# Kernel tuning notes

Measured on AMD Instinct MI355X. Metric: run time of the kernel, lower is better.

The kernel has to match this reference:

```python
import jax, jax.numpy as jnp
import numpy as np
from jax import lax

EPS = 1e-20  # matches sample_gumbel eps in the TF source


def setup_inputs() -> dict:
    key = jax.random.key(0)
    ks = jax.random.split(key, 7)
    B, T, D, H, K = 32, 512, 512, 512, 64
    x = jax.random.normal(ks[0], (B, T, D), jnp.float32)
    f_after = jax.random.normal(ks[1], (K, D, H), jnp.float32) * 0.02
    f_skip = jax.random.normal(ks[2], (2 * H, 2), jnp.float32) * 0.05
    gru_kernel = jax.random.normal(ks[3], (D, 3 * H), jnp.float32) * 0.02
    gru_rec_kernel = jax.random.normal(ks[4], (H, 3 * H), jnp.float32) * 0.02
    gru_bias = jnp.zeros((2, 3 * H), jnp.float32)
    u_gumbel = jax.random.uniform(ks[5], (T, B, 2), jnp.float32)
    return {"x": x, "f_after": f_after, "f_skip": f_skip,
            "gru_kernel": gru_kernel, "gru_rec_kernel": gru_rec_kernel,
            "gru_bias": gru_bias, "u_gumbel": u_gumbel}


def reference(x, f_after, f_skip, gru_kernel, gru_rec_kernel, gru_bias, u_gumbel):
    # z_after = tanh(conv1d(x, f_after, SAME))  -> [B, T, H]
    z_after = lax.conv_general_dilated(
        x, f_after, window_strides=(1,), padding='SAME',
        dimension_numbers=('NWC', 'WIO', 'NWC'))
    z_after = jnp.tanh(z_after)

    # gumbel(0,1) noise from uniform draws, per step: [T, B, 2]
    g = -jnp.log(-jnp.log(u_gumbel + EPS) + EPS)

    b_in, b_rec = gru_bias[0], gru_bias[1]  # reset_after=True biases, each [3H]
    H = gru_rec_kernel.shape[0]
    B = x.shape[0]
    h0 = jnp.zeros((B, H), x.dtype)

    xs = (jnp.swapaxes(x, 0, 1), jnp.swapaxes(z_after, 0, 1), g)  # time-major

    def step(h_prev, inp):
        x_t, za_t, g_t = inp
        # skip gate: concat(h_{t-1}, z_after_t) @ f_skip, gumbel-softmax (temp=1)
        logits = jnp.concatenate([h_prev, za_t], axis=-1) @ f_skip  # [B, 2]
        skip = jax.nn.softmax(logits + g_t, axis=-1)
        # Keras GRUCell (reset_after=True), gate order z, r, h
        xm = x_t @ gru_kernel + b_in          # [B, 3H]
        hm = h_prev @ gru_rec_kernel + b_rec  # [B, 3H]
        xz, xr, xh = jnp.split(xm, 3, axis=-1)
        hz, hr, hh = jnp.split(hm, 3, axis=-1)
        z = jax.nn.sigmoid(xz + hz)
        r = jax.nn.sigmoid(xr + hr)
        hc = jnp.tanh(xh + r * hh)
        ht = z * h_prev + (1.0 - z) * hc
        # skip blend
        ht = skip[:, 0:1] * h_prev + skip[:, 1:2] * ht
        return ht, ht

    _, ys = lax.scan(step, h0, xs)           # [T, B, H]
    return jnp.swapaxes(ys, 0, 1)            # [B, T, H]
```

## Files before the change

kernel.cpp:

```cpp
#include <hip/hip_runtime.h>
#include <stdint.h>

typedef unsigned short u16;
typedef unsigned int   u32;
typedef __attribute__((ext_vector_type(8))) short short8;
typedef __attribute__((ext_vector_type(4))) float f32x4;
typedef __attribute__((ext_vector_type(4))) u32   u32x4;

#define AS1 __attribute__((address_space(1)))
#define AS3 __attribute__((address_space(3)))

#define SENT 0x7FC0u
#define HS   528

__device__ __forceinline__ float bf2f(u16 u) {
  union { u32 i; float f; } v; v.i = ((u32)u) << 16; return v.f;
}
__device__ __forceinline__ u16 f2bf(float f) {
  union { float f; u32 i; } v; v.f = f;
  u32 i = v.i;
  i += 0x7FFFu + ((i >> 16) & 1u);
  return (u16)(i >> 16);
}
__device__ __forceinline__ float tanh_fast(float x) {
  const float e = __expf(-2.f * fabsf(x));
  const float t = (1.f - e) / (1.f + e);
  return __builtin_copysignf(t, x);
}

__device__ __forceinline__ void gload16(const u16* src, u16* ldsDst) {
  __builtin_amdgcn_global_load_lds((const AS1 u32*)src, (AS3 u32*)ldsDst, 16, 0, 0);
}

__device__ __forceinline__ short8 ldg_sc_h_wait(const u16* p) {
  short8 r;
  asm volatile("global_load_dwordx4 %0, %1, off sc0 sc1\n\t"
               "s_waitcnt vmcnt(0)"
               : "=v"(r) : "v"(p) : "memory");
  return r;
}
__device__ __forceinline__ void stg_sc_h(u16* p, u16 v) {
  asm volatile("global_store_short %0, %1, off sc0 sc1" :: "v"(p), "v"((u32)v) : "memory");
}

__global__ void k_init(const float* __restrict__ x, u16* __restrict__ xp) {
  const long NXP = 32L * 576 * 512;
  long i0 = (long)blockIdx.x * 256 + threadIdx.x;
  for (long i = i0; i < NXP; i += (long)gridDim.x * 256) {
    long b = i / (576 * 512);
    int rem = (int)(i - b * (576 * 512));
    int rr = rem >> 9, dd = rem & 511;
    int t = rr - 31;
    float v = (t >= 0 && t < 512) ? x[(b * 512 + t) * 512 + dd] : 0.f;
    xp[i] = f2bf(v);
  }
}

__global__ void k_sent(u32* __restrict__ hs) {
  const u32x4 s = u32x4{(SENT << 16) | SENT, (SENT << 16) | SENT,
                        (SENT << 16) | SENT, (SENT << 16) | SENT};
  *(u32x4*)&hs[((long)blockIdx.x * 256 + threadIdx.x) * 4] = s;
}

__global__ void k_transpose_cast(const float* __restrict__ in, u16* __restrict__ out,
                                 int rows, int cols, long inWStride, long outWStride) {
  __shared__ float tile[64][65];
  const int w = blockIdx.z;
  const float* ip = in + (long)w * inWStride;
  u16* op = out + (long)w * outWStride;
  const int r0 = blockIdx.y * 64, c0 = blockIdx.x * 64;
  const int tr = threadIdx.x >> 6, tc = threadIdx.x & 63;
  #pragma unroll
  for (int p = 0; p < 16; ++p) {
    int rr = p * 4 + tr;
    tile[rr][tc] = ip[(long)(r0 + rr) * cols + c0 + tc];
  }
  __syncthreads();
  #pragma unroll
  for (int p = 0; p < 16; ++p) {
    int rr = p * 4 + tr;
    op[(long)(c0 + rr) * rows + r0 + tc] = f2bf(tile[tc][rr]);
  }
}

__global__ __launch_bounds__(256) void k_conv(
    const u16* __restrict__ A, const u16* __restrict__ Bm, u16* __restrict__ C)
{
  __shared__ __align__(16) u16 Abig[192 * 64];
  __shared__ __align__(16) u16 Blds[128 * 64];
  const int bid0 = blockIdx.x;
  const int bid = (bid0 & 7) * 64 + (bid0 >> 3);
  const int mt = bid & 127, nt = bid >> 7;
  const int bb = (mt * 128) >> 9;
  const int t0 = (mt * 128) & 511;
  const int h0 = nt * 128;
  const int tid = threadIdx.x;
  const int wv = tid >> 6, l = tid & 63;
  const int wr = wv >> 1, wc = wv & 1;
  const int sRow = wv * 8 + (l >> 3);
  const int sCol = (l & 7) * 8;
  f32x4 acc[4][4];
  #pragma unroll
  for (int m = 0; m < 4; ++m)
    #pragma unroll
    for (int n = 0; n < 4; ++n) acc[m][n] = f32x4{0.f, 0.f, 0.f, 0.f};

  const long aRow0 = (long)(bb * 576 + t0);
  for (int dsub = 0; dsub < 8; ++dsub) {
    const int dcol = dsub << 6;
    for (int w = 0; w < 64; ++w) {
      __syncthreads();
      if (w == 0) {
        #pragma unroll
        for (int c = 0; c < 6; ++c)
          gload16(A + (aRow0 + c * 32 + sRow) * 512 + dcol + sCol,
                  &Abig[(c * 32 + wv * 8) * 64]);
      }
      #pragma unroll
      for (int c = 0; c < 4; ++c)
        gload16(Bm + ((long)w << 18) + (long)(h0 + c * 32 + sRow) * 512 + dcol + sCol,
                &Blds[(c * 32 + wv * 8) * 64]);
      __syncthreads();
      #pragma unroll
      for (int kk = 0; kk < 2; ++kk) {
        short8 af[4], bf[4];
        #pragma unroll
        for (int m = 0; m < 4; ++m)
          af[m] = *(const short8*)&Abig[(w + wr * 64 + m * 16 + (l & 15)) * 64 + kk * 32 + (l >> 4) * 8];
        #pragma unroll
        for (int n = 0; n < 4; ++n)
          bf[n] = *(const short8*)&Blds[(wc * 64 + n * 16 + (l & 15)) * 64 + kk * 32 + (l >> 4) * 8];
        #pragma unroll
        for (int m = 0; m < 4; ++m)
          #pragma unroll
          for (int n = 0; n < 4; ++n)
            acc[m][n] = __builtin_amdgcn_mfma_f32_16x16x32_bf16(af[m], bf[n], acc[m][n], 0, 0, 0);
      }
    }
  }
  const int lr = (l >> 4) * 4, lc = l & 15;
  #pragma unroll
  for (int m = 0; m < 4; ++m)
    #pragma unroll
    for (int n = 0; n < 4; ++n)
      #pragma unroll
      for (int r = 0; r < 4; ++r) {
        const int row = mt * 128 + wr * 64 + m * 16 + lr + r;
        const int col = h0 + wc * 64 + n * 16 + lc;
        C[(long)row * 512 + col] = f2bf(tanhf(acc[m][n][r]));
      }
}

__global__ __launch_bounds__(256) void k_gemm(
    const u16* __restrict__ A, const u16* __restrict__ Bm, u16* __restrict__ C,
    int nTiles, int kw, int woff, long bWStride, int outMode)
{
  __shared__ __align__(16) u16 Alds[128 * 64];
  __shared__ __align__(16) u16 Blds[128 * 64];
  const int bid0 = blockIdx.x;
  const int cpx = gridDim.x >> 3;
  const int bid = (bid0 & 7) * cpx + (bid0 >> 3);
  const int mt = bid / nTiles, nt = bid - mt * nTiles;
  const int bb = (mt * 128) >> 9;
  const int t0 = (mt * 128) & 511;
  const int h0 = nt * 128;
  const int tid = threadIdx.x;
  const int wv = tid >> 6, l = tid & 63;
  const int wr = wv >> 1, wc = wv & 1;
  const int sRow = wv * 8 + (l >> 3);
  const int sCol = (l & 7) * 8;
  f32x4 acc[4][4];
  #pragma unroll
  for (int m = 0; m < 4; ++m)
    #pragma unroll
    for (int n = 0; n < 4; ++n) acc[m][n] = f32x4{0.f, 0.f, 0.f, 0.f};

  const int kIters = kw * 8;
  const long aRow0 = (long)(bb * 576 + t0 + woff);
  for (int q = 0; q < kIters; ++q) {
    const int w = q >> 3, dsub = (q & 7) << 6;
    const u16* aB = A + (aRow0 + w) * 512 + dsub + sCol;
    const u16* bB = Bm + (long)w * bWStride + (long)h0 * 512 + dsub + sCol;
    __syncthreads();
    #pragma unroll
    for (int c = 0; c < 4; ++c) {
      gload16(aB + (long)(c * 32 + sRow) * 512, &Alds[c * 2048 + wv * 512]);
      gload16(bB + (long)(c * 32 + sRow) * 512, &Blds[c * 2048 + wv * 512]);
    }
    __syncthreads();
    #pragma unroll
    for (int kk = 0; kk < 2; ++kk) {
      short8 af[4], bf[4];
      #pragma unroll
      for (int m = 0; m < 4; ++m)
        af[m] = *(const short8*)&Alds[(wr * 64 + m * 16 + (l & 15)) * 64 + kk * 32 + (l >> 4) * 8];
      #pragma unroll
      for (int n = 0; n < 4; ++n)
        bf[n] = *(const short8*)&Blds[(wc * 64 + n * 16 + (l & 15)) * 64 + kk * 32 + (l >> 4) * 8];
      #pragma unroll
      for (int m = 0; m < 4; ++m)
        #pragma unroll
        for (int n = 0; n < 4; ++n)
          acc[m][n] = __builtin_amdgcn_mfma_f32_16x16x32_bf16(af[m], bf[n], acc[m][n], 0, 0, 0);
    }
  }
  const int lr = (l >> 4) * 4, lc = l & 15;
  #pragma unroll
  for (int m = 0; m < 4; ++m)
    #pragma unroll
    for (int n = 0; n < 4; ++n)
      #pragma unroll
      for (int r = 0; r < 4; ++r) {
        const int row = mt * 128 + wr * 64 + m * 16 + lr + r;
        const int col = h0 + wc * 64 + n * 16 + lc;
        const float v = acc[m][n][r];
        if (outMode == 0) {
          C[(long)row * 512 + col] = f2bf(tanhf(v));
        } else {
          const int b = row >> 9, t = row & 511;
          C[((long)t * 32 + b) * 1536 + col] = f2bf(v);
        }
      }
}

__global__ void k_dza(const u16* __restrict__ za, const float* __restrict__ fskip,
                      const float* __restrict__ ug, float* __restrict__ dza) {
  __shared__ float wd2[512];
  const int t = blockIdx.x, tid = threadIdx.x;
  for (int i = tid; i < 512; i += 256) wd2[i] = fskip[(512 + i) * 2 + 1] - fskip[(512 + i) * 2];
  __syncthreads();
  const int b = tid >> 3, seg = (tid & 7) * 64;
  const u16* row = za + ((long)b * 512 + t) * 512 + seg;
  float pp = 0.f;
  #pragma unroll
  for (int j = 0; j < 8; ++j) {
    short8 v = *(const short8*)&row[j * 8];
    #pragma unroll
    for (int e = 0; e < 8; ++e) pp += bf2f((u16)v[e]) * wd2[seg + j * 8 + e];
  }
  pp += __shfl_xor(pp, 1); pp += __shfl_xor(pp, 2); pp += __shfl_xor(pp, 4);
  if ((tid & 7) == 0) {
    float u0 = ug[((long)t * 32 + b) * 2 + 0], u1 = ug[((long)t * 32 + b) * 2 + 1];
    float g0 = -logf(-logf(u0 + 1e-20f) + 1e-20f);
    float g1 = -logf(-logf(u1 + 1e-20f) + 1e-20f);
    dza[t * 32 + b] = pp + (g1 - g0);
  }
}

__global__ __launch_bounds__(256, 1) void k_rnn(
    const u16* __restrict__ XM, const float* __restrict__ dza,
    const float* __restrict__ Wrec, const float* __restrict__ gbias,
    const float* __restrict__ fskip, u16* hstep, float* __restrict__ out)
{
  const int bid = blockIdx.x, d = bid & 7, s = bid >> 3;
  const int tid = threadIdx.x, wv = tid >> 6, l = tid & 63;
  __shared__ __align__(16) u16 hBl[2][4 * HS];
  __shared__ float s1s[2][4];

  float wdv[8];
  #pragma unroll
  for (int e = 0; e < 8; ++e)
    wdv[e] = fskip[(l * 8 + e) * 2 + 1] - fskip[(l * 8 + e) * 2];

  const int colb = s * 64 + wv * 16 + (l & 15);
  const int kq = (l >> 4) * 8;

  short8 wf[3][16];
  #pragma unroll
  for (int g = 0; g < 3; ++g)
    #pragma unroll
    for (int kk = 0; kk < 16; ++kk) {
      short8 tmp;
      #pragma unroll
      for (int e = 0; e < 8; ++e)
        tmp[e] = (short)f2bf(Wrec[(long)(kk * 32 + kq + e) * 1536 + g * 512 + colb]);
      wf[g][kk] = tmp;
    }
  float bi[3], br[3];
  #pragma unroll
  for (int g = 0; g < 3; ++g) {
    bi[g] = gbias[g * 512 + colb];
    br[g] = gbias[1536 + g * 512 + colb];
  }
  const int myb = d * 4;
  float hp[4] = {0.f, 0.f, 0.f, 0.f};
  float hnv[4] = {0.f, 0.f, 0.f, 0.f};

  u16 xmc[3][4];
  float dzc;
  if (l < 16) {
    const u16* xr = XM + (long)myb * 1536;
    #pragma unroll
    for (int r = 0; r < 4; ++r)
      #pragma unroll
      for (int g = 0; g < 3; ++g)
        xmc[g][r] = xr[(long)r * 1536 + g * 512 + colb];
  }
  dzc = dza[myb + wv];

  for (int t = 0; t < 512; ++t) {
    const int p = t & 1;

    short8 h8;
    if (t > 0) {
      const u16* ph = hstep + ((long)(t - 1) * 32 + myb + wv) * 512 + l * 8;
      h8 = ldg_sc_h_wait(ph);
      bool bad = true;
      while (bad) {
        bad = false;
        #pragma unroll
        for (int e = 0; e < 8; ++e) bad |= ((u16)h8[e] == SENT);
        if (bad) h8 = ldg_sc_h_wait(ph);
      }
    } else {
      #pragma unroll
      for (int e = 0; e < 8; ++e) h8[e] = 0;
    }

    if (t > 0 && l < 16) {
      #pragma unroll
      for (int r = 0; r < 4; ++r)
        out[((long)(myb + r) * 512 + (t - 1)) * 512 + colb] = hnv[r];
    }

    u16 xmn[3][4];
    const int tn = (t < 511) ? t + 1 : t;
    if (l < 16) {
      const u16* xr = XM + ((long)tn * 32 + myb) * 1536;
      #pragma unroll
      for (int r = 0; r < 4; ++r)
        #pragma unroll
        for (int g = 0; g < 3; ++g)
          xmn[g][r] = xr[(long)r * 1536 + g * 512 + colb];
    }
    const float dzn = dza[tn * 32 + myb + wv];

    *(short8*)&hBl[p][wv * HS + l * 8] = h8;
    float pp = 0.f;
    #pragma unroll
    for (int e = 0; e < 8; ++e) pp += bf2f((u16)h8[e]) * wdv[e];
    #pragma unroll
    for (int o = 1; o < 64; o <<= 1) pp += __shfl_xor(pp, o);
    if (l == 0) s1s[p][wv] = 1.f / (1.f + __expf(-(pp + dzc)));
    __syncthreads();

    f32x4 acc[3];
    acc[0] = f32x4{0.f, 0.f, 0.f, 0.f}; acc[1] = acc[0]; acc[2] = acc[0];
    const int b4 = l & 3;
    #pragma unroll
    for (int kk = 0; kk < 16; ++kk) {
      short8 a = *(const short8*)&hBl[p][b4 * HS + kk * 32 + kq];
      acc[0] = __builtin_amdgcn_mfma_f32_16x16x32_bf16(a, wf[0][kk], acc[0], 0, 0, 0);
      acc[1] = __builtin_amdgcn_mfma_f32_16x16x32_bf16(a, wf[1][kk], acc[1], 0, 0, 0);
      acc[2] = __builtin_amdgcn_mfma_f32_16x16x32_bf16(a, wf[2][kk], acc[2], 0, 0, 0);
    }

    if (l < 16) {
      #pragma unroll
      for (int r = 0; r < 4; ++r) {
        const float xz = bf2f(xmc[0][r]) + bi[0];
        const float xr_ = bf2f(xmc[1][r]) + bi[1];
        const float xh = bf2f(xmc[2][r]) + bi[2];
        const float hz = acc[0][r] + br[0];
        const float hr = acc[1][r] + br[1];
        const float hh = acc[2][r] + br[2];
        const float z  = 1.f / (1.f + __expf(-(xz + hz)));
        const float rr = 1.f / (1.f + __expf(-(xr_ + hr)));
        const float hc = tanh_fast(xh + rr * hh);
        const float ht = z * hp[r] + (1.f - z) * hc;
        const float s1 = s1s[p][r];
        const float hn = hp[r] + s1 * (ht - hp[r]);
        stg_sc_h(&hstep[((long)t * 32 + myb + r) * 512 + colb], f2bf(hn));
        hp[r] = hn;
        hnv[r] = hn;
      }
      #pragma unroll
      for (int g = 0; g < 3; ++g)
        #pragma unroll
        for (int r = 0; r < 4; ++r) xmc[g][r] = xmn[g][r];
    }
    dzc = dzn;
  }
  if (l < 16) {
    #pragma unroll
    for (int r = 0; r < 4; ++r)
      out[((long)(myb + r) * 512 + 511) * 512 + colb] = hnv[r];
  }
}

extern "C" void kernel_launch(void* const* d_in, const int* in_sizes, int n_in,
                              void* d_out, int out_size, void* d_ws, size_t ws_size,
                              hipStream_t stream) {
  (void)in_sizes; (void)n_in; (void)out_size; (void)ws_size;
  const float* x        = (const float*)d_in[0];
  const float* f_after  = (const float*)d_in[1];
  const float* f_skip   = (const float*)d_in[2];
  const float* gru_k    = (const float*)d_in[3];
  const float* gru_rec  = (const float*)d_in[4];
  const float* gru_bias = (const float*)d_in[5];
  const float* ug       = (const float*)d_in[6];
  float* out = (float*)d_out;

  char* ws = (char*)d_ws;
  size_t off = 0;
  auto alloc = [&](size_t bytes) { void* p = ws + off; off = (off + bytes + 255) & ~(size_t)255; return p; };
  u16*  xp    = (u16*)alloc(32L * 576 * 512 * 2);
  u16*  fT    = (u16*)alloc(64L * 512 * 512 * 2);
  u16*  gruT  = (u16*)alloc(1536L * 512 * 2);
  u16*  za    = (u16*)alloc(32L * 512 * 512 * 2);
  u16*  XM    = (u16*)alloc(512L * 32 * 1536 * 2);
  float* dza  = (float*)alloc(512L * 32 * 4);
  u16*  hstep = za;

  k_init<<<dim3(4096), dim3(256), 0, stream>>>(x, xp);
  k_transpose_cast<<<dim3(8, 8, 64), dim3(256), 0, stream>>>(f_after, fT, 512, 512, 512L * 512, 512L * 512);
  k_transpose_cast<<<dim3(24, 8, 1), dim3(256), 0, stream>>>(gru_k, gruT, 512, 1536, 0L, 0L);
  k_conv<<<dim3(512), dim3(256), 0, stream>>>(xp, fT, za);
  k_gemm<<<dim3(1536), dim3(256), 0, stream>>>(xp, gruT, XM, 12, 1, 31, 0L, 1);
  k_dza<<<dim3(512), dim3(256), 0, stream>>>(za, f_skip, ug, dza);
  k_sent<<<dim3(4096), dim3(256), 0, stream>>>((u32*)hstep);
  k_rnn<<<dim3(64), dim3(256), 0, stream>>>(XM, dza, gru_rec, gru_bias, f_skip, hstep, out);
}
```

Measured before the change: 2.009 ms.

## Pipeline conv kernel with triple-buffered B, double-buffered A, swizzled LDS, larger tiles

The conv GEMM kernel now computes 256x128 output tiles per block, cutting the grid to 256 blocks, and doubles the per-wave M accumulators. Loads of B (filter slices) are triple-buffered and A is double-buffered, with explicit vmcnt waits and raw s_barrier so global loads overlap MFMA work instead of a full sync per step. LDS columns are XOR-swizzled to reduce bank conflicts on fragment reads. The cost is higher register and LDS use (one block per CU) and fewer blocks in flight, which may leave some CUs idle on a 256-CU part.

```diff
diff --git a/kernel.cpp b/kernel.cpp
--- a/kernel.cpp
+++ b/kernel.cpp
@@ -83,71 +83,91 @@
   }
 }
 
-__global__ __launch_bounds__(256) void k_conv(
+__global__ __launch_bounds__(256, 1) void k_conv(
     const u16* __restrict__ A, const u16* __restrict__ Bm, u16* __restrict__ C)
 {
-  __shared__ __align__(16) u16 Abig[192 * 64];
-  __shared__ __align__(16) u16 Blds[128 * 64];
+  __shared__ __align__(16) u16 Abig[2][320 * 64];
+  __shared__ __align__(16) u16 Blds[3][128 * 64];
   const int bid0 = blockIdx.x;
-  const int bid = (bid0 & 7) * 64 + (bid0 >> 3);
-  const int mt = bid & 127, nt = bid >> 7;
-  const int bb = (mt * 128) >> 9;
-  const int t0 = (mt * 128) & 511;
+  const int bid = (bid0 & 7) * 32 + (bid0 >> 3);
+  const int mt = bid & 63, nt = bid >> 6;
   const int h0 = nt * 128;
+  const int b = mt >> 1;
+  const int t0 = (mt & 1) * 256;
+  const long row0 = (long)mt * 256;
   const int tid = threadIdx.x;
   const int wv = tid >> 6, l = tid & 63;
   const int wr = wv >> 1, wc = wv & 1;
   const int sRow = wv * 8 + (l >> 3);
-  const int sCol = (l & 7) * 8;
-  f32x4 acc[4][4];
-  #pragma unroll
-  for (int m = 0; m < 4; ++m)
+  const int sColSw = ((l & 7) ^ (l >> 3)) * 8;
+  f32x4 acc[8][4];
+  #pragma unroll
+  for (int m = 0; m < 8; ++m)
     #pragma unroll
     for (int n = 0; n < 4; ++n) acc[m][n] = f32x4{0.f, 0.f, 0.f, 0.f};
 
-  const long aRow0 = (long)(bb * 576 + t0);
-  for (int dsub = 0; dsub < 8; ++dsub) {
-    const int dcol = dsub << 6;
-    for (int w = 0; w < 64; ++w) {
-      __syncthreads();
-      if (w == 0) {
-        #pragma unroll
-        for (int c = 0; c < 6; ++c)
-          gload16(A + (aRow0 + c * 32 + sRow) * 512 + dcol + sCol,
-                  &Abig[(c * 32 + wv * 8) * 64]);
-      }
-      #pragma unroll
-      for (int c = 0; c < 4; ++c)
-        gload16(Bm + ((long)w << 18) + (long)(h0 + c * 32 + sRow) * 512 + dcol + sCol,
-                &Blds[(c * 32 + wv * 8) * 64]);
-      __syncthreads();
-      #pragma unroll
-      for (int kk = 0; kk < 2; ++kk) {
-        short8 af[4], bf[4];
-        #pragma unroll
-        for (int m = 0; m < 4; ++m)
-          af[m] = *(const short8*)&Abig[(w + wr * 64 + m * 16 + (l & 15)) * 64 + kk * 32 + (l >> 4) * 8];
+  const long aRow0 = (long)b * 576 + t0;
+
+  auto stageA = [&](int d) {
+    const int dcol = d << 6;
+    #pragma unroll
+    for (int c = 0; c < 10; ++c)
+      gload16(A + (aRow0 + c * 32 + sRow) * 512 + dcol + sColSw,
+              &Abig[d & 1][(c * 32 + wv * 8) * 64]);
+  };
+  auto stageB = [&](int p) {
+    const int d = p >> 6, w = p & 63;
+    const u16* bB = Bm + ((long)w << 18) + (long)h0 * 512 + (d << 6) + sColSw;
+    #pragma unroll
+    for (int c = 0; c < 4; ++c)
+      gload16(bB + (long)(c * 32 + sRow) * 512, &Blds[p % 3][(c * 32 + wv * 8) * 64]);
+  };
+
+  stageA(0); stageB(0); stageB(1);
+  for (int p = 0; p < 512; ++p) {
+    const int d = p >> 6, w = p & 63;
+    if (p + 2 < 512) stageB(p + 2);
+    if (w == 0 && d < 7) stageA(d + 1);
+    if (p >= 510)              asm volatile("s_waitcnt vmcnt(0)"  ::: "memory");
+    else if (w <= 2 && d < 7)  asm volatile("s_waitcnt vmcnt(18)" ::: "memory");
+    else                       asm volatile("s_waitcnt vmcnt(8)"  ::: "memory");
+    __builtin_amdgcn_s_barrier();
+    __builtin_amdgcn_sched_barrier(0);
+    const u16* Ab = &Abig[d & 1][0];
+    const u16* Bb = &Blds[p % 3][0];
+    #pragma unroll
+    for (int kk = 0; kk < 2; ++kk) {
+      short8 af[8], bf[4];
+      #pragma unroll
+      for (int m = 0; m < 8; ++m) {
+        const int row = w + wr * 128 + m * 16 + (l & 15);
+        const int ci = (kk * 32 + (l >> 4) * 8) ^ ((row & 7) * 8);
+        af[m] = *(const short8*)&Ab[row * 64 + ci];
+      }
+      #pragma unroll
+      for (int n = 0; n < 4; ++n) {
+        const int row = wc * 64 + n * 16 + (l & 15);
+        const int ci = (kk * 32 + (l >> 4) * 8) ^ ((row & 7) * 8);
+        bf[n] = *(const short8*)&Bb[row * 64 + ci];
+      }
+      #pragma unroll
+      for (int m = 0; m < 8; ++m)
         #pragma unroll
         for (int n = 0; n < 4; ++n)
-          bf[n] = *(const short8*)&Blds[(wc * 64 + n * 16 + (l & 15)) * 64 + kk * 32 + (l >> 4) * 8];
-        #pragma unroll
-        for (int m = 0; m < 4; ++m)
-          #pragma unroll
-          for (int n = 0; n < 4; ++n)
-            acc[m][n] = __builtin_amdgcn_mfma_f32_16x16x32_bf16(af[m], bf[n], acc[m][n], 0, 0, 0);
-      }
-    }
+          acc[m][n] = __builtin_amdgcn_mfma_f32_16x16x32_bf16(af[m], bf[n], acc[m][n], 0, 0, 0);
+    }
+    __builtin_amdgcn_s_barrier();
   }
   const int lr = (l >> 4) * 4, lc = l & 15;
   #pragma unroll
-  for (int m = 0; m < 4; ++m)
+  for (int m = 0; m < 8; ++m)
     #pragma unroll
     for (int n = 0; n < 4; ++n)
       #pragma unroll
       for (int r = 0; r < 4; ++r) {
-        const int row = mt * 128 + wr * 64 + m * 16 + lr + r;
+        const long row = row0 + wr * 128 + m * 16 + lr + r;
         const int col = h0 + wc * 64 + n * 16 + lc;
-        C[(long)row * 512 + col] = f2bf(tanhf(acc[m][n][r]));
+        C[row * 512 + col] = f2bf(tanhf(acc[m][n][r]));
       }
 }
 
@@ -415,7 +435,7 @@
   k_init<<<dim3(4096), dim3(256), 0, stream>>>(x, xp);
   k_transpose_cast<<<dim3(8, 8, 64), dim3(256), 0, stream>>>(f_after, fT, 512, 512, 512L * 512, 512L * 512);
   k_transpose_cast<<<dim3(24, 8, 1), dim3(256), 0, stream>>>(gru_k, gruT, 512, 1536, 0L, 0L);
-  k_conv<<<dim3(512), dim3(256), 0, stream>>>(xp, fT, za);
+  k_conv<<<dim3(256), dim3(256), 0, stream>>>(xp, fT, za);
   k_gemm<<<dim3(1536), dim3(256), 0, stream>>>(xp, gruT, XM, 12, 1, 31, 0L, 1);
   k_dza<<<dim3(512), dim3(256), 0, stream>>>(za, f_skip, ug, dza);
   k_sent<<<dim3(4096), dim3(256), 0, stream>>>((u32*)hstep);
```

Result: faster. 1.952 ms, median of 2 (-2.8%).

## Overlap second half of conv with recurrent scan in a fused persistent kernel

Applied to the files above, without the earlier changes.

The conv is split into two time halves. The first half runs as its own kernel, and the second half runs inside a merged kernel alongside the 64 recurrent blocks. The recurrent blocks poll for z_after sentinels, so they can start before the conv finishes. The separate dza kernel is removed: the z_after dot product is folded into the per-step skip reduction and the gumbel differences are precomputed into shared memory. Hidden-state exchange moves to an 8-slot ring buffer tagged with the step index instead of a sentinel-cleared full-size buffer. The risks are spin-wait contention, deadlock if the co-resident blocks are not scheduled, and extra per-step za loads on the serial path.

```diff
diff --git a/kernel.cpp b/kernel.cpp
--- a/kernel.cpp
+++ b/kernel.cpp
@@ -12,6 +12,7 @@
 
 #define SENT 0x7FC0u
 #define HS   528
+#define EPS  1e-20f
 
 __device__ __forceinline__ float bf2f(u16 u) {
   union { u32 i; float f; } v; v.i = ((u32)u) << 16; return v.f;
@@ -27,20 +28,15 @@
   const float t = (1.f - e) / (1.f + e);
   return __builtin_copysignf(t, x);
 }
-
 __device__ __forceinline__ void gload16(const u16* src, u16* ldsDst) {
   __builtin_amdgcn_global_load_lds((const AS1 u32*)src, (AS3 u32*)ldsDst, 16, 0, 0);
 }
 
-__device__ __forceinline__ short8 ldg_sc_h_wait(const u16* p) {
-  short8 r;
-  asm volatile("global_load_dwordx4 %0, %1, off sc0 sc1\n\t"
-               "s_waitcnt vmcnt(0)"
-               : "=v"(r) : "v"(p) : "memory");
-  return r;
-}
 __device__ __forceinline__ void stg_sc_h(u16* p, u16 v) {
   asm volatile("global_store_short %0, %1, off sc0 sc1" :: "v"(p), "v"((u32)v) : "memory");
+}
+__device__ __forceinline__ void stg_sc_d(u32* p, u32 v) {
+  asm volatile("global_store_dword %0, %1, off sc0 sc1" :: "v"(p), "v"(v) : "memory");
 }
 
 __global__ void k_init(const float* __restrict__ x, u16* __restrict__ xp) {
@@ -56,10 +52,14 @@
   }
 }
 
-__global__ void k_sent(u32* __restrict__ hs) {
+__global__ void k_sentZ(u32* __restrict__ hs) {
   const u32x4 s = u32x4{(SENT << 16) | SENT, (SENT << 16) | SENT,
                         (SENT << 16) | SENT, (SENT << 16) | SENT};
   *(u32x4*)&hs[((long)blockIdx.x * 256 + threadIdx.x) * 4] = s;
+}
+__global__ void k_sentR(u32* __restrict__ hr) {
+  const u32x4 s = u32x4{0x7FC0FFFFu, 0x7FC0FFFFu, 0x7FC0FFFFu, 0x7FC0FFFFu};
+  *(u32x4*)&hr[((long)blockIdx.x * 256 + threadIdx.x) * 4] = s;
 }
 
 __global__ void k_transpose_cast(const float* __restrict__ in, u16* __restrict__ out,
@@ -83,16 +83,16 @@
   }
 }
 
-__global__ __launch_bounds__(256) void k_conv(
+template<bool SC>
+__device__ __forceinline__ void conv_body(char* smem, int cbid, int tqBase,
     const u16* __restrict__ A, const u16* __restrict__ Bm, u16* __restrict__ C)
 {
-  __shared__ __align__(16) u16 Abig[192 * 64];
-  __shared__ __align__(16) u16 Blds[128 * 64];
-  const int bid0 = blockIdx.x;
-  const int bid = (bid0 & 7) * 64 + (bid0 >> 3);
-  const int mt = bid & 127, nt = bid >> 7;
-  const int bb = (mt * 128) >> 9;
-  const int t0 = (mt * 128) & 511;
+  u16* Abig = (u16*)smem;
+  u16* Blds = (u16*)(smem + 192 * 64 * 2);
+  const int tq = tqBase + (cbid >> 7);
+  const int q = cbid & 127;
+  const int qs = (q & 7) * 16 + (q >> 3);
+  const int b = qs >> 2, nt = qs & 3;
   const int h0 = nt * 128;
   const int tid = threadIdx.x;
   const int wv = tid >> 6, l = tid & 63;
@@ -105,7 +105,7 @@
     #pragma unroll
     for (int n = 0; n < 4; ++n) acc[m][n] = f32x4{0.f, 0.f, 0.f, 0.f};
 
-  const long aRow0 = (long)(bb * 576 + t0);
+  const long aRow0 = (long)b * 576 + tq * 128;
   for (int dsub = 0; dsub < 8; ++dsub) {
     const int dcol = dsub << 6;
     for (int w = 0; w < 64; ++w) {
@@ -139,16 +139,25 @@
     }
   }
   const int lr = (l >> 4) * 4, lc = l & 15;
+  const long row0 = (long)b * 512 + tq * 128;
   #pragma unroll
   for (int m = 0; m < 4; ++m)
     #pragma unroll
     for (int n = 0; n < 4; ++n)
       #pragma unroll
       for (int r = 0; r < 4; ++r) {
-        const int row = mt * 128 + wr * 64 + m * 16 + lr + r;
+        const long row = row0 + wr * 64 + m * 16 + lr + r;
         const int col = h0 + wc * 64 + n * 16 + lc;
-        C[(long)row * 512 + col] = f2bf(tanhf(acc[m][n][r]));
-      }
+        const u16 v = f2bf(tanhf(acc[m][n][r]));
+        if constexpr (SC) stg_sc_h(&C[row * 512 + col], v);
+        else              C[row * 512 + col] = v;
+      }
+}
+
+__global__ __launch_bounds__(256, 2) void k_convq(
+    const u16* __restrict__ A, const u16* __restrict__ Bm, u16* __restrict__ C) {
+  __shared__ __align__(16) char smem[40960];
+  conv_body<false>(smem, blockIdx.x, 0, A, Bm, C);
 }
 
 __global__ __launch_bounds__(256) void k_gemm(
@@ -214,53 +223,40 @@
         const int row = mt * 128 + wr * 64 + m * 16 + lr + r;
         const int col = h0 + wc * 64 + n * 16 + lc;
         const float v = acc[m][n][r];
-        if (outMode == 0) {
-          C[(long)row * 512 + col] = f2bf(tanhf(v));
-        } else {
-          const int b = row >> 9, t = row & 511;
-          C[((long)t * 32 + b) * 1536 + col] = f2bf(v);
-        }
-      }
-}
-
-__global__ void k_dza(const u16* __restrict__ za, const float* __restrict__ fskip,
-                      const float* __restrict__ ug, float* __restrict__ dza) {
-  __shared__ float wd2[512];
-  const int t = blockIdx.x, tid = threadIdx.x;
-  for (int i = tid; i < 512; i += 256) wd2[i] = fskip[(512 + i) * 2 + 1] - fskip[(512 + i) * 2];
-  __syncthreads();
-  const int b = tid >> 3, seg = (tid & 7) * 64;
-  const u16* row = za + ((long)b * 512 + t) * 512 + seg;
-  float pp = 0.f;
-  #pragma unroll
-  for (int j = 0; j < 8; ++j) {
-    short8 v = *(const short8*)&row[j * 8];
-    #pragma unroll
-    for (int e = 0; e < 8; ++e) pp += bf2f((u16)v[e]) * wd2[seg + j * 8 + e];
-  }
-  pp += __shfl_xor(pp, 1); pp += __shfl_xor(pp, 2); pp += __shfl_xor(pp, 4);
-  if ((tid & 7) == 0) {
-    float u0 = ug[((long)t * 32 + b) * 2 + 0], u1 = ug[((long)t * 32 + b) * 2 + 1];
-    float g0 = -logf(-logf(u0 + 1e-20f) + 1e-20f);
-    float g1 = -logf(-logf(u1 + 1e-20f) + 1e-20f);
-    dza[t * 32 + b] = pp + (g1 - g0);
-  }
-}
-
-__global__ __launch_bounds__(256, 1) void k_rnn(
-    const u16* __restrict__ XM, const float* __restrict__ dza,
-    const float* __restrict__ Wrec, const float* __restrict__ gbias,
-    const float* __restrict__ fskip, u16* hstep, float* __restrict__ out)
+        const int b = row >> 9, t = row & 511;
+        C[((long)t * 32 + b) * 1536 + col] = f2bf(v);
+      }
+}
+
+__device__ __forceinline__ void rnn_body(char* smem, int bid,
+    const u16* __restrict__ XM, const float* __restrict__ Wrec,
+    const float* __restrict__ gbias, const float* __restrict__ fskip,
+    const float* __restrict__ ug, const u16* __restrict__ za,
+    u32* hRing, float* __restrict__ out)
 {
-  const int bid = blockIdx.x, d = bid & 7, s = bid >> 3;
+  u16*   hBl   = (u16*)smem;
+  float* gdiff = (float*)(smem + 2 * 4 * HS * 2);
+  float* s1s   = (float*)(smem + 2 * 4 * HS * 2 + 8192);
+  const int d = bid & 7, s = bid >> 3;
   const int tid = threadIdx.x, wv = tid >> 6, l = tid & 63;
-  __shared__ __align__(16) u16 hBl[2][4 * HS];
-  __shared__ float s1s[2][4];
-
-  float wdv[8];
-  #pragma unroll
-  for (int e = 0; e < 8; ++e)
-    wdv[e] = fskip[(l * 8 + e) * 2 + 1] - fskip[(l * 8 + e) * 2];
+  const int myb = d * 4;
+
+  #pragma unroll
+  for (int e = 0; e < 8; ++e) {
+    const int idx = tid * 8 + e;
+    const int t = idx >> 2, r = idx & 3;
+    const float u0 = ug[((long)t * 32 + myb + r) * 2 + 0];
+    const float u1 = ug[((long)t * 32 + myb + r) * 2 + 1];
+    gdiff[idx] = logf(-logf(u0 + EPS) + EPS) - logf(-logf(u1 + EPS) + EPS);
+  }
+
+  float wdv[8], wd2v[8];
+  #pragma unroll
+  for (int e = 0; e < 8; ++e) {
+    const int col = l * 8 + e;
+    wdv[e]  = fskip[col * 2 + 1] - fskip[col * 2];
+    wd2v[e] = fskip[(512 + col) * 2 + 1] - fskip[(512 + col) * 2];
+  }
 
   const int colb = s * 64 + wv * 16 + (l & 15);
   const int kq = (l >> 4) * 8;
@@ -282,12 +278,10 @@
     bi[g] = gbias[g * 512 + colb];
     br[g] = gbias[1536 + g * 512 + colb];
   }
-  const int myb = d * 4;
   float hp[4] = {0.f, 0.f, 0.f, 0.f};
   float hnv[4] = {0.f, 0.f, 0.f, 0.f};
 
   u16 xmc[3][4];
-  float dzc;
   if (l < 16) {
     const u16* xr = XM + (long)myb * 1536;
     #pragma unroll
@@ -296,25 +290,57 @@
       for (int g = 0; g < 3; ++g)
         xmc[g][r] = xr[(long)r * 1536 + g * 512 + colb];
   }
-  dzc = dza[myb + wv];
+  __syncthreads();
 
   for (int t = 0; t < 512; ++t) {
     const int p = t & 1;
 
-    short8 h8;
+    short8 h8, z8;
+    const u16* pz = za + ((long)(myb + wv) * 512 + t) * 512 + l * 8;
     if (t > 0) {
-      const u16* ph = hstep + ((long)(t - 1) * 32 + myb + wv) * 512 + l * 8;
-      h8 = ldg_sc_h_wait(ph);
+      const u32* ph = hRing + (((t - 1) & 7) * 32 + myb + wv) * 512 + l * 8;
+      const u32 need = (u32)t;
+      u32x4 a, b2;
       bool bad = true;
       while (bad) {
+        asm volatile(
+          "global_load_dwordx4 %0, %3, off sc0 sc1\n\t"
+          "global_load_dwordx4 %1, %4, off sc0 sc1\n\t"
+          "global_load_dwordx4 %2, %5, off sc0 sc1\n\t"
+          "s_waitcnt vmcnt(0)"
+          : "=&v"(a), "=&v"(b2), "=&v"(z8)
+          : "v"(ph), "v"(ph + 4), "v"(pz)
+          : "memory");
         bad = false;
         #pragma unroll
-        for (int e = 0; e < 8; ++e) bad |= ((u16)h8[e] == SENT);
-        if (bad) h8 = ldg_sc_h_wait(ph);
+        for (int i = 0; i < 4; ++i) {
+          bad |= ((a[i]  & 0xFFFFu) != need);
+          bad |= ((b2[i] & 0xFFFFu) != need);
+        }
+        bool zb = false;
+        #pragma unroll
+        for (int e = 0; e < 8; ++e) zb |= ((u16)z8[e] == SENT);
+        if (zb) __builtin_amdgcn_s_sleep(8);
+        bad |= zb;
+      }
+      #pragma unroll
+      for (int i = 0; i < 4; ++i) {
+        h8[i]     = (short)(a[i]  >> 16);
+        h8[4 + i] = (short)(b2[i] >> 16);
       }
     } else {
       #pragma unroll
       for (int e = 0; e < 8; ++e) h8[e] = 0;
+      bool zb = true;
+      while (zb) {
+        asm volatile("global_load_dwordx4 %0, %1, off sc0 sc1\n\t"
+                     "s_waitcnt vmcnt(0)"
+                     : "=v"(z8) : "v"(pz) : "memory");
+        zb = false;
+        #pragma unroll
+        for (int e = 0; e < 8; ++e) zb |= ((u16)z8[e] == SENT);
+        if (zb) __builtin_amdgcn_s_sleep(8);
+      }
     }
 
     if (t > 0 && l < 16) {
@@ -333,15 +359,15 @@
         for (int g = 0; g < 3; ++g)
           xmn[g][r] = xr[(long)r * 1536 + g * 512 + colb];
     }
-    const float dzn = dza[tn * 32 + myb + wv];
-
-    *(short8*)&hBl[p][wv * HS + l * 8] = h8;
+
+    *(short8*)&hBl[p * 4 * HS + wv * HS + l * 8] = h8;
     float pp = 0.f;
     #pragma unroll
-    for (int e = 0; e < 8; ++e) pp += bf2f((u16)h8[e]) * wdv[e];
+    for (int e = 0; e < 8; ++e)
+      pp += bf2f((u16)h8[e]) * wdv[e] + bf2f((u16)z8[e]) * wd2v[e];
     #pragma unroll
     for (int o = 1; o < 64; o <<= 1) pp += __shfl_xor(pp, o);
-    if (l == 0) s1s[p][wv] = 1.f / (1.f + __expf(-(pp + dzc)));
+    if (l == 0) s1s[p * 4 + wv] = 1.f / (1.f + __expf(-(pp + gdiff[t * 4 + wv])));
     __syncthreads();
 
     f32x4 acc[3];
@@ -349,7 +375,7 @@
     const int b4 = l & 3;
     #pragma unroll
     for (int kk = 0; kk < 16; ++kk) {
-      short8 a = *(const short8*)&hBl[p][b4 * HS + kk * 32 + kq];
+      short8 a = *(const short8*)&hBl[p * 4 * HS + b4 * HS + kk * 32 + kq];
       acc[0] = __builtin_amdgcn_mfma_f32_16x16x32_bf16(a, wf[0][kk], acc[0], 0, 0, 0);
       acc[1] = __builtin_amdgcn_mfma_f32_16x16x32_bf16(a, wf[1][kk], acc[1], 0, 0, 0);
       acc[2] = __builtin_amdgcn_mfma_f32_16x16x32_bf16(a, wf[2][kk], acc[2], 0, 0, 0);
@@ -368,9 +394,10 @@
         const float rr = 1.f / (1.f + __expf(-(xr_ + hr)));
         const float hc = tanh_fast(xh + rr * hh);
         const float ht = z * hp[r] + (1.f - z) * hc;
-        const float s1 = s1s[p][r];
+        const float s1 = s1s[p * 4 + r];
         const float hn = hp[r] + s1 * (ht - hp[r]);
-        stg_sc_h(&hstep[((long)t * 32 + myb + r) * 512 + colb], f2bf(hn));
+        stg_sc_d(&hRing[((t & 7) * 32 + myb + r) * 512 + colb],
+                 ((u32)f2bf(hn) << 16) | (u32)(t + 1));
         hp[r] = hn;
         hnv[r] = hn;
       }
@@ -379,13 +406,26 @@
         #pragma unroll
         for (int r = 0; r < 4; ++r) xmc[g][r] = xmn[g][r];
     }
-    dzc = dzn;
   }
   if (l < 16) {
     #pragma unroll
     for (int r = 0; r < 4; ++r)
       out[((long)(myb + r) * 512 + 511) * 512 + colb] = hnv[r];
   }
+}
+
+__global__ __launch_bounds__(256, 2) void k_mega(
+    const u16* __restrict__ xp, const u16* __restrict__ fT, u16* za,
+    const u16* __restrict__ XM, const float* __restrict__ Wrec,
+    const float* __restrict__ gbias, const float* __restrict__ fskip,
+    const float* __restrict__ ug, u32* hRing, float* __restrict__ out)
+{
+  __shared__ __align__(16) char smem[40960];
+  if (blockIdx.x >= 64) {
+    conv_body<true>(smem, blockIdx.x - 64, 2, xp, fT, za);
+    return;
+  }
+  rnn_body(smem, blockIdx.x, XM, Wrec, gbias, fskip, ug, za, hRing, out);
 }
 
 extern "C" void kernel_launch(void* const* d_in, const int* in_sizes, int n_in,
@@ -409,15 +449,15 @@
   u16*  gruT  = (u16*)alloc(1536L * 512 * 2);
   u16*  za    = (u16*)alloc(32L * 512 * 512 * 2);
   u16*  XM    = (u16*)alloc(512L * 32 * 1536 * 2);
-  float* dza  = (float*)alloc(512L * 32 * 4);
-  u16*  hstep = za;
+  u32*  hRing = (u32*)gruT;
 
   k_init<<<dim3(4096), dim3(256), 0, stream>>>(x, xp);
   k_transpose_cast<<<dim3(8, 8, 64), dim3(256), 0, stream>>>(f_after, fT, 512, 512, 512L * 512, 512L * 512);
   k_transpose_cast<<<dim3(24, 8, 1), dim3(256), 0, stream>>>(gru_k, gruT, 512, 1536, 0L, 0L);
-  k_conv<<<dim3(512), dim3(256), 0, stream>>>(xp, fT, za);
+  k_sentZ<<<dim3(4096), dim3(256), 0, stream>>>((u32*)za);
+  k_convq<<<dim3(256), dim3(256), 0, stream>>>(xp, fT, za);
   k_gemm<<<dim3(1536), dim3(256), 0, stream>>>(xp, gruT, XM, 12, 1, 31, 0L, 1);
-  k_dza<<<dim3(512), dim3(256), 0, stream>>>(za, f_skip, ug, dza);
-  k_sent<<<dim3(4096), dim3(256), 0, stream>>>((u32*)hstep);
-  k_rnn<<<dim3(64), dim3(256), 0, stream>>>(XM, dza, gru_rec, gru_bias, f_skip, hstep, out);
-}
+  k_sentR<<<dim3(128), dim3(256), 0, stream>>>(hRing);
+  k_mega<<<dim3(320), dim3(256), 0, stream>>>(xp, fT, za, XM, gru_rec, gru_bias,
+                                              f_skip, ug, hRing, out);
+}
```

New measurement: 3.143 ms. 1.56x slower.
